# Optimization experiments

Hardware: AMD Instinct MI355X
Metric: run time of the kernel (lower is better)

The kernel has to match this reference:

```python
import jax, jax.numpy as jnp
import numpy as np

N_DET, N_T, NY, NX, B = 128, 2048, 256, 256, 4


def setup_inputs() -> dict:
    key = jax.random.key(0)
    k1, k2, k3 = jax.random.split(key, 3)
    sino = jax.random.normal(k1, (B, 1, N_DET, N_T), dtype=jnp.float32)
    # lut[..., 0]: fractional time-of-flight index in [0, n_t-1)
    tof = jax.random.uniform(k2, (NY, NX, N_DET), dtype=jnp.float32) * (N_T - 1)
    # lut[..., 1]: linear-interp fraction alpha in [0, 1)
    alpha = jax.random.uniform(k3, (NY, NX, N_DET), dtype=jnp.float32)
    lut = jnp.stack([tof, alpha], axis=-1)  # [ny, nx, n_det, 2]
    return {"sino": sino, "lut": lut}


def reference(sino, lut):
    b, _, n_det, n_t = sino.shape
    ny, nx = lut.shape[0], lut.shape[1]
    P = ny * nx

    # Precompute (as in __init__): floor index, validity mask, interp fraction.
    k_floor = jnp.floor(lut[..., 0])
    valid = (k_floor >= 0) & (k_floor < n_t - 1)
    k0 = jnp.clip(k_floor, 0, max(n_t - 2, 0)).astype(jnp.int32)  # [ny,nx,n_det]
    alpha = lut[..., 1]

    # Hann apodization window over detectors (non-trainable buffer).
    apod = (0.5 - 0.5 * jnp.cos(
        2.0 * jnp.pi * jnp.arange(n_det, dtype=jnp.float32) / max(n_det - 1, 1)
    )).astype(sino.dtype)

    S = sino[:, 0]  # [B, n_det, n_t]

    # Move detector axis first so we can gather all detectors at once.
    k0t = k0.reshape(P, n_det).T          # [n_det, P]
    at = alpha.reshape(P, n_det).T        # [n_det, P]
    vt = valid.reshape(P, n_det).T.astype(sino.dtype)  # [n_det, P]

    s0 = jnp.take_along_axis(S, k0t[None], axis=2)        # [B, n_det, P]
    s1 = jnp.take_along_axis(S, (k0t + 1)[None], axis=2)  # [B, n_det, P]
    sk = ((1.0 - at) * s0 + at * s1) * vt                  # masked lerp

    out = jnp.einsum('d,bdp->bp', apod, sk)                # apodized reduce over detectors
    norm = jnp.maximum(apod.sum(), jnp.finfo(apod.dtype).tiny)
    return (out / norm).reshape(b, 1, ny, nx)
```

## Files before the change

### kernel.cpp

```cpp
#include <hip/hip_runtime.h>
#include <hip/hip_fp16.h>

#define N_DET 128
#define N_T   2048
#define NPIX  65536
#define NBATCH 4
#define G 4
#define NGRP (N_DET / G)
#define TPX 2048
#define NTILE (NPIX / TPX)
#define PXT 4

typedef float f4_t __attribute__((ext_vector_type(4)));

__global__ __launch_bounds__(256) void sino_pack_kernel(
    const float* __restrict__ sino, float2* __restrict__ ws,
    float* __restrict__ out) {
  const int idx = blockIdx.x * blockDim.x + threadIdx.x;
  const __half2 lo = __floats2half2_rn(
      __builtin_nontemporal_load(sino + 0 * N_DET * N_T + idx),
      __builtin_nontemporal_load(sino + 1 * N_DET * N_T + idx));
  const __half2 hi = __floats2half2_rn(
      __builtin_nontemporal_load(sino + 2 * N_DET * N_T + idx),
      __builtin_nontemporal_load(sino + 3 * N_DET * N_T + idx));
  union { struct { __half2 a, b; } h; float2 f; } u;
  u.h.a = lo;
  u.h.b = hi;
  ws[idx] = u.f;
  out[idx] = 0.0f;
}

__global__ __launch_bounds__(512, 4) void das_lds_kernel(
    const float* __restrict__ lut, const float2* __restrict__ ws,
    float* __restrict__ out) {
  __shared__ __align__(16) float2 sbuf[G][N_T];

  const int id = blockIdx.x;
  const int T = ((id >> 8) << 3) | (id & 7);
  const int g = (id >> 3) & 31;
  const int tid = threadIdx.x;

  f4_t l[PXT][2];
  const char* lb = reinterpret_cast<const char*>(lut);
#pragma unroll
  for (int i = 0; i < PXT; ++i) {
    const size_t P = (size_t)T * TPX + i * 512 + tid;
    const f4_t* lp = reinterpret_cast<const f4_t*>(lb + P * (N_DET * 8) +
                                                   (size_t)g * (G * 8));
    l[i][0] = lp[0];
    l[i][1] = lp[1];
  }

  {
    const char* src = reinterpret_cast<const char*>(ws) + (size_t)g * 65536;
    char* dstb = reinterpret_cast<char*>(&sbuf[0][0]);
#pragma unroll
    for (int r = 0; r < 8; ++r) {
      __builtin_amdgcn_global_load_lds(
          (const __attribute__((address_space(1))) void*)(src + r * 8192 +
                                                          tid * 16),
          (__attribute__((address_space(3))) void*)(dstb + r * 8192 + tid * 16),
          16, 0, 0);
    }
  }

  float apd[G];
#pragma unroll
  for (int dd = 0; dd < G; ++dd)
    apd[dd] = 0.5f - 0.5f * cosf(6.28318530717958647692f *
                                 ((float)(g * G + dd) / 127.0f));

  __syncthreads();

  float4 acc[PXT];
#pragma unroll
  for (int i = 0; i < PXT; ++i) acc[i] = make_float4(0.f, 0.f, 0.f, 0.f);

#pragma unroll
  for (int i = 0; i < PXT; ++i) {
#pragma unroll
    for (int dd = 0; dd < G; ++dd) {
      const float tof = (dd & 1) ? l[i][dd >> 1].z : l[i][dd >> 1].x;
      const float al  = (dd & 1) ? l[i][dd >> 1].w : l[i][dd >> 1].y;
      const float kf = floorf(tof);
      const bool valid = (kf >= 0.0f) && (kf < (float)(N_T - 1));
      const int k0 = (int)fminf(fmaxf(kf, 0.0f), (float)(N_T - 2));
      const float w = valid ? apd[dd] : 0.0f;

      const float2 r0 = sbuf[dd][k0];
      const float2 r1 = sbuf[dd][k0 + 1];
      const __half2* h0 = reinterpret_cast<const __half2*>(&r0);
      const __half2* h1 = reinterpret_cast<const __half2*>(&r1);
      const float2 s0a = __half22float2(h0[0]);
      const float2 s0b = __half22float2(h0[1]);
      const float2 s1a = __half22float2(h1[0]);
      const float2 s1b = __half22float2(h1[1]);

      acc[i].x += w * (s0a.x + al * (s1a.x - s0a.x));
      acc[i].y += w * (s0a.y + al * (s1a.y - s0a.y));
      acc[i].z += w * (s0b.x + al * (s1b.x - s0b.x));
      acc[i].w += w * (s0b.y + al * (s1b.y - s0b.y));
    }
  }

  const float nrm = 1.0f / 63.5f;
#pragma unroll
  for (int i = 0; i < PXT; ++i) {
    const int P = T * TPX + i * 512 + tid;
    atomicAdd(out + 0 * NPIX + P, acc[i].x * nrm);
    atomicAdd(out + 1 * NPIX + P, acc[i].y * nrm);
    atomicAdd(out + 2 * NPIX + P, acc[i].z * nrm);
    atomicAdd(out + 3 * NPIX + P, acc[i].w * nrm);
  }
}

__global__ __launch_bounds__(256) void das_fallback_kernel(
    const float* __restrict__ lut, const float* __restrict__ S,
    float* __restrict__ out) {
  const int lane = threadIdx.x & 63;
  const int p = blockIdx.x * 4 + (threadIdx.x >> 6);

  const float4 lv =
      reinterpret_cast<const float4*>(lut + (size_t)p * 2 * N_DET)[lane];

  float acc0 = 0.f, acc1 = 0.f, acc2 = 0.f, acc3 = 0.f;
  float wsum = 0.f;

#pragma unroll
  for (int j = 0; j < 2; ++j) {
    const int d = 2 * lane + j;
    const float tof = j ? lv.z : lv.x;
    const float a   = j ? lv.w : lv.y;
    const float kf = floorf(tof);
    const bool valid = (kf >= 0.0f) && (kf < (float)(N_T - 1));
    const float kcl = fminf(fmaxf(kf, 0.0f), (float)(N_T - 2));
    const int k0 = (int)kcl;
    const float apd =
        0.5f - 0.5f * cosf(6.28318530717958647692f *
                           (1.0f / (float)(N_DET - 1)) * (float)d);
    wsum += apd;
    const float w = valid ? apd : 0.0f;
    const float om = 1.0f - a;
    const float* row = S + (size_t)d * N_T + k0;
    acc0 += w * (om * row[0 * N_DET * N_T] + a * row[0 * N_DET * N_T + 1]);
    acc1 += w * (om * row[1 * N_DET * N_T] + a * row[1 * N_DET * N_T + 1]);
    acc2 += w * (om * row[2 * N_DET * N_T] + a * row[2 * N_DET * N_T + 1]);
    acc3 += w * (om * row[3 * N_DET * N_T] + a * row[3 * N_DET * N_T + 1]);
  }

#pragma unroll
  for (int off = 32; off > 0; off >>= 1) {
    acc0 += __shfl_xor(acc0, off);
    acc1 += __shfl_xor(acc1, off);
    acc2 += __shfl_xor(acc2, off);
    acc3 += __shfl_xor(acc3, off);
    wsum += __shfl_xor(wsum, off);
  }

  if (lane == 0) {
    const float inv = 1.0f / fmaxf(wsum, 1.17549435e-38f);
    out[0 * NPIX + p] = acc0 * inv;
    out[1 * NPIX + p] = acc1 * inv;
    out[2 * NPIX + p] = acc2 * inv;
    out[3 * NPIX + p] = acc3 * inv;
  }
}

extern "C" void kernel_launch(void* const* d_in, const int* in_sizes, int n_in,
                              void* d_out, int out_size, void* d_ws, size_t ws_size,
                              hipStream_t stream) {
  const float* sino = (const float*)d_in[0];
  const float* lut  = (const float*)d_in[1];
  float* out = (float*)d_out;

  const size_t need = (size_t)N_DET * N_T * 8;
  if (ws_size >= need) {
    float2* ws = (float2*)d_ws;
    sino_pack_kernel<<<(N_DET * N_T) / 256, 256, 0, stream>>>(sino, ws, out);
    das_lds_kernel<<<NTILE * NGRP, 512, 0, stream>>>(lut, ws, out);
  } else {
    das_fallback_kernel<<<NPIX / 4, 256, 0, stream>>>(lut, sino, out);
  }
}
```

Before: 123.7 us.

## Enlarge pixel tiles per block and prefetch next LUT slice in-loop

Halves the number of pixel tiles so each block loads its detector-group sinogram slab into LDS once and reuses it across 8 pixel iterations instead of 4. The LUT loads are now software-pipelined: the next iteration's LUT values are fetched while the current one is being computed. Atomics are issued per iteration instead of being held in a large accumulator array. The aim is to cut redundant LDS staging traffic and register pressure. The cost is half as many blocks (512), which lowers the parallelism available to hide latency on the memory-bound LUT stream.

```diff
diff --git a/kernel.cpp b/kernel.cpp
--- a/kernel.cpp
+++ b/kernel.cpp
@@ -7,9 +7,10 @@
 #define NBATCH 4
 #define G 4
 #define NGRP (N_DET / G)
-#define TPX 2048
-#define NTILE (NPIX / TPX)
-#define PXT 4
+#define NTILE 16
+#define TPX (NPIX / NTILE)
+#define THREADS 512
+#define IPT (TPX / THREADS)
 
 typedef float f4_t __attribute__((ext_vector_type(4)));
 
@@ -35,21 +36,17 @@
     float* __restrict__ out) {
   __shared__ __align__(16) float2 sbuf[G][N_T];
 
-  const int id = blockIdx.x;
-  const int T = ((id >> 8) << 3) | (id & 7);
-  const int g = (id >> 3) & 31;
+  const int b = blockIdx.x;
+  const int T = ((b >> 8) << 3) | (b & 7);
+  const int g = (b >> 3) & 31;
   const int tid = threadIdx.x;
 
-  f4_t l[PXT][2];
-  const char* lb = reinterpret_cast<const char*>(lut);
-#pragma unroll
-  for (int i = 0; i < PXT; ++i) {
-    const size_t P = (size_t)T * TPX + i * 512 + tid;
-    const f4_t* lp = reinterpret_cast<const f4_t*>(lb + P * (N_DET * 8) +
-                                                   (size_t)g * (G * 8));
-    l[i][0] = lp[0];
-    l[i][1] = lp[1];
-  }
+  const char* lb = reinterpret_cast<const char*>(lut) +
+                   ((size_t)(T * TPX + tid) * (N_DET * 8)) + (size_t)g * (G * 8);
+  const size_t istride = (size_t)THREADS * (N_DET * 8);
+
+  f4_t lc0 = reinterpret_cast<const f4_t*>(lb)[0];
+  f4_t lc1 = reinterpret_cast<const f4_t*>(lb)[1];
 
   {
     const char* src = reinterpret_cast<const char*>(ws) + (size_t)g * 65536;
@@ -72,16 +69,23 @@
 
   __syncthreads();
 
-  float4 acc[PXT];
-#pragma unroll
-  for (int i = 0; i < PXT; ++i) acc[i] = make_float4(0.f, 0.f, 0.f, 0.f);
+  const float nrm = 1.0f / 63.5f;
 
 #pragma unroll
-  for (int i = 0; i < PXT; ++i) {
+  for (int i = 0; i < IPT; ++i) {
+    f4_t ln0, ln1;
+    if (i + 1 < IPT) {
+      const f4_t* lp = reinterpret_cast<const f4_t*>(lb + (size_t)(i + 1) * istride);
+      ln0 = lp[0];
+      ln1 = lp[1];
+    }
+
+    float ax = 0.f, ay = 0.f, az = 0.f, aw = 0.f;
 #pragma unroll
     for (int dd = 0; dd < G; ++dd) {
-      const float tof = (dd & 1) ? l[i][dd >> 1].z : l[i][dd >> 1].x;
-      const float al  = (dd & 1) ? l[i][dd >> 1].w : l[i][dd >> 1].y;
+      const f4_t& lv = (dd < 2) ? lc0 : lc1;
+      const float tof = (dd & 1) ? lv.z : lv.x;
+      const float al  = (dd & 1) ? lv.w : lv.y;
       const float kf = floorf(tof);
       const bool valid = (kf >= 0.0f) && (kf < (float)(N_T - 1));
       const int k0 = (int)fminf(fmaxf(kf, 0.0f), (float)(N_T - 2));
@@ -96,21 +100,20 @@
       const float2 s1a = __half22float2(h1[0]);
       const float2 s1b = __half22float2(h1[1]);
 
-      acc[i].x += w * (s0a.x + al * (s1a.x - s0a.x));
-      acc[i].y += w * (s0a.y + al * (s1a.y - s0a.y));
-      acc[i].z += w * (s0b.x + al * (s1b.x - s0b.x));
-      acc[i].w += w * (s0b.y + al * (s1b.y - s0b.y));
+      ax += w * (s0a.x + al * (s1a.x - s0a.x));
+      ay += w * (s0a.y + al * (s1a.y - s0a.y));
+      az += w * (s0b.x + al * (s1b.x - s0b.x));
+      aw += w * (s0b.y + al * (s1b.y - s0b.y));
     }
-  }
 
-  const float nrm = 1.0f / 63.5f;
-#pragma unroll
-  for (int i = 0; i < PXT; ++i) {
-    const int P = T * TPX + i * 512 + tid;
-    atomicAdd(out + 0 * NPIX + P, acc[i].x * nrm);
-    atomicAdd(out + 1 * NPIX + P, acc[i].y * nrm);
-    atomicAdd(out + 2 * NPIX + P, acc[i].z * nrm);
-    atomicAdd(out + 3 * NPIX + P, acc[i].w * nrm);
+    const int P = T * TPX + i * THREADS + tid;
+    atomicAdd(out + 0 * NPIX + P, ax * nrm);
+    atomicAdd(out + 1 * NPIX + P, ay * nrm);
+    atomicAdd(out + 2 * NPIX + P, az * nrm);
+    atomicAdd(out + 3 * NPIX + P, aw * nrm);
+
+    lc0 = ln0;
+    lc1 = ln1;
   }
 }
 
@@ -177,7 +180,7 @@
   if (ws_size >= need) {
     float2* ws = (float2*)d_ws;
     sino_pack_kernel<<<(N_DET * N_T) / 256, 256, 0, stream>>>(sino, ws, out);
-    das_lds_kernel<<<NTILE * NGRP, 512, 0, stream>>>(lut, ws, out);
+    das_lds_kernel<<<NGRP * NTILE, THREADS, 0, stream>>>(lut, ws, out);
   } else {
     das_fallback_kernel<<<NPIX / 4, 256, 0, stream>>>(lut, sino, out);
   }
```

Result: slower. 139.1 us (+12.5%).

## Double-buffer LDS sinogram staging across 16-detector chunks per block

Applied to the files above, without the earlier changes.

Each block now owns 1024 pixels and a 16-detector chunk instead of 2048 pixels and 4 detectors. It streams pairs of detector rows into two alternating LDS buffers, so the next pair loads while the current pair is interpolated. This cuts the atomicAdd count per pixel by a factor of four and spreads LDS fills over the work instead of one up-front load. In exchange it adds a barrier per phase, uses 16 LUT vector registers per thread, and has less pixel parallelism per block.

```diff
diff --git a/kernel.cpp b/kernel.cpp
--- a/kernel.cpp
+++ b/kernel.cpp
@@ -5,11 +5,14 @@
 #define N_T   2048
 #define NPIX  65536
 #define NBATCH 4
-#define G 4
-#define NGRP (N_DET / G)
-#define TPX 2048
+#define THREADS 512
+#define PXT 2
+#define TPX (THREADS * PXT)
 #define NTILE (NPIX / TPX)
-#define PXT 4
+#define CDET 16
+#define NCB (N_DET / CDET)
+#define GR 2
+#define PHASES (CDET / GR)
 
 typedef float f4_t __attribute__((ext_vector_type(4)));
 
@@ -33,42 +36,43 @@
 __global__ __launch_bounds__(512, 4) void das_lds_kernel(
     const float* __restrict__ lut, const float2* __restrict__ ws,
     float* __restrict__ out) {
-  __shared__ __align__(16) float2 sbuf[G][N_T];
-
-  const int id = blockIdx.x;
-  const int T = ((id >> 8) << 3) | (id & 7);
-  const int g = (id >> 3) & 31;
+  __shared__ __align__(16) float2 sbuf[2][GR * N_T];
+
+  const int b = blockIdx.x;
+  const int T = b >> 3;
+  const int c = b & 7;
   const int tid = threadIdx.x;
 
-  f4_t l[PXT][2];
-  const char* lb = reinterpret_cast<const char*>(lut);
+  f4_t l[PXT][PHASES];
 #pragma unroll
   for (int i = 0; i < PXT; ++i) {
-    const size_t P = (size_t)T * TPX + i * 512 + tid;
-    const f4_t* lp = reinterpret_cast<const f4_t*>(lb + P * (N_DET * 8) +
-                                                   (size_t)g * (G * 8));
-    l[i][0] = lp[0];
-    l[i][1] = lp[1];
-  }
-
-  {
-    const char* src = reinterpret_cast<const char*>(ws) + (size_t)g * 65536;
-    char* dstb = reinterpret_cast<char*>(&sbuf[0][0]);
-#pragma unroll
-    for (int r = 0; r < 8; ++r) {
+    const size_t P = (size_t)T * TPX + i * THREADS + tid;
+    const f4_t* lp =
+        reinterpret_cast<const f4_t*>(lut + (P * N_DET + c * CDET) * 2);
+#pragma unroll
+    for (int j = 0; j < PHASES; ++j) l[i][j] = lp[j];
+  }
+
+  auto stage = [&](int p, int bf) {
+    const char* src = reinterpret_cast<const char*>(ws) +
+                      ((size_t)(c * CDET + GR * p) << 14);
+    char* dst = reinterpret_cast<char*>(&sbuf[bf][0]);
+#pragma unroll
+    for (int r = 0; r < 4; ++r) {
       __builtin_amdgcn_global_load_lds(
           (const __attribute__((address_space(1))) void*)(src + r * 8192 +
                                                           tid * 16),
-          (__attribute__((address_space(3))) void*)(dstb + r * 8192 + tid * 16),
+          (__attribute__((address_space(3))) void*)(dst + r * 8192 + tid * 16),
           16, 0, 0);
     }
-  }
-
-  float apd[G];
-#pragma unroll
-  for (int dd = 0; dd < G; ++dd)
-    apd[dd] = 0.5f - 0.5f * cosf(6.28318530717958647692f *
-                                 ((float)(g * G + dd) / 127.0f));
+  };
+  stage(0, 0);
+
+  asm volatile(""
+               : "+v"(l[0][0]), "+v"(l[0][1]), "+v"(l[0][2]), "+v"(l[0][3]),
+                 "+v"(l[0][4]), "+v"(l[0][5]), "+v"(l[0][6]), "+v"(l[0][7]),
+                 "+v"(l[1][0]), "+v"(l[1][1]), "+v"(l[1][2]), "+v"(l[1][3]),
+                 "+v"(l[1][4]), "+v"(l[1][5]), "+v"(l[1][6]), "+v"(l[1][7]));
 
   __syncthreads();
 
@@ -77,36 +81,51 @@
   for (int i = 0; i < PXT; ++i) acc[i] = make_float4(0.f, 0.f, 0.f, 0.f);
 
 #pragma unroll
+  for (int p = 0; p < PHASES; ++p) {
+    if (p + 1 < PHASES) stage(p + 1, (p + 1) & 1);
+
+    const int d0 = c * CDET + GR * p;
+    const float apd0 =
+        0.5f - 0.5f * cosf(6.28318530717958647692f * ((float)d0 / 127.0f));
+    const float apd1 = 0.5f - 0.5f * cosf(6.28318530717958647692f *
+                                          ((float)(d0 + 1) / 127.0f));
+
+    const float2* sb = &sbuf[p & 1][0];
+#pragma unroll
+    for (int i = 0; i < PXT; ++i) {
+      const f4_t lv = l[i][p];
+#pragma unroll
+      for (int r = 0; r < GR; ++r) {
+        const float tof = r ? lv.z : lv.x;
+        const float al  = r ? lv.w : lv.y;
+        const float kf = floorf(tof);
+        const bool valid = (kf >= 0.0f) && (kf < (float)(N_T - 1));
+        const int k0 = (int)fminf(fmaxf(kf, 0.0f), (float)(N_T - 2));
+        const float w = valid ? (r ? apd1 : apd0) : 0.0f;
+
+        const float2 r0 = sb[r * N_T + k0];
+        const float2 r1 = sb[r * N_T + k0 + 1];
+        const __half2* h0 = reinterpret_cast<const __half2*>(&r0);
+        const __half2* h1 = reinterpret_cast<const __half2*>(&r1);
+        const float2 s0a = __half22float2(h0[0]);
+        const float2 s0b = __half22float2(h0[1]);
+        const float2 s1a = __half22float2(h1[0]);
+        const float2 s1b = __half22float2(h1[1]);
+
+        acc[i].x += w * (s0a.x + al * (s1a.x - s0a.x));
+        acc[i].y += w * (s0a.y + al * (s1a.y - s0a.y));
+        acc[i].z += w * (s0b.x + al * (s1b.x - s0b.x));
+        acc[i].w += w * (s0b.y + al * (s1b.y - s0b.y));
+      }
+    }
+
+    if (p + 1 < PHASES) __syncthreads();
+  }
+
+  const float nrm = 1.0f / 63.5f;
+#pragma unroll
   for (int i = 0; i < PXT; ++i) {
-#pragma unroll
-    for (int dd = 0; dd < G; ++dd) {
-      const float tof = (dd & 1) ? l[i][dd >> 1].z : l[i][dd >> 1].x;
-      const float al  = (dd & 1) ? l[i][dd >> 1].w : l[i][dd >> 1].y;
-      const float kf = floorf(tof);
-      const bool valid = (kf >= 0.0f) && (kf < (float)(N_T - 1));
-      const int k0 = (int)fminf(fmaxf(kf, 0.0f), (float)(N_T - 2));
-      const float w = valid ? apd[dd] : 0.0f;
-
-      const float2 r0 = sbuf[dd][k0];
-      const float2 r1 = sbuf[dd][k0 + 1];
-      const __half2* h0 = reinterpret_cast<const __half2*>(&r0);
-      const __half2* h1 = reinterpret_cast<const __half2*>(&r1);
-      const float2 s0a = __half22float2(h0[0]);
-      const float2 s0b = __half22float2(h0[1]);
-      const float2 s1a = __half22float2(h1[0]);
-      const float2 s1b = __half22float2(h1[1]);
-
-      acc[i].x += w * (s0a.x + al * (s1a.x - s0a.x));
-      acc[i].y += w * (s0a.y + al * (s1a.y - s0a.y));
-      acc[i].z += w * (s0b.x + al * (s1b.x - s0b.x));
-      acc[i].w += w * (s0b.y + al * (s1b.y - s0b.y));
-    }
-  }
-
-  const float nrm = 1.0f / 63.5f;
-#pragma unroll
-  for (int i = 0; i < PXT; ++i) {
-    const int P = T * TPX + i * 512 + tid;
+    const int P = T * TPX + i * THREADS + tid;
     atomicAdd(out + 0 * NPIX + P, acc[i].x * nrm);
     atomicAdd(out + 1 * NPIX + P, acc[i].y * nrm);
     atomicAdd(out + 2 * NPIX + P, acc[i].z * nrm);
@@ -177,7 +196,7 @@
   if (ws_size >= need) {
     float2* ws = (float2*)d_ws;
     sino_pack_kernel<<<(N_DET * N_T) / 256, 256, 0, stream>>>(sino, ws, out);
-    das_lds_kernel<<<NTILE * NGRP, 512, 0, stream>>>(lut, ws, out);
+    das_lds_kernel<<<NTILE * NCB, THREADS, 0, stream>>>(lut, ws, out);
   } else {
     das_fallback_kernel<<<NPIX / 4, 256, 0, stream>>>(lut, sino, out);
   }
```

New measurement: 161.5 us. +30.5%, slower.
